# Kernel tuning notes

Hardware: AMD Instinct MI355X
Metric: run time of the kernel (lower is better)

## Reference

```python
import jax, jax.numpy as jnp
import numpy as np

N = 100000      # nodes
E = 1600000     # edges (before self loops)
IN_C, HID_C, OUT_C = 128, 64, 40


def setup_inputs() -> dict:
    key = jax.random.key(0)
    k = jax.random.split(key, 6)
    x = jax.random.normal(k[0], (N, IN_C), dtype=jnp.float32)
    edge_index = jax.random.randint(k[1], (2, E), 0, N, dtype=jnp.int64)
    W1 = jax.random.normal(k[2], (IN_C, HID_C), dtype=jnp.float32) * (1.0 / np.sqrt(IN_C))
    b1 = jnp.zeros((HID_C,), jnp.float32)
    W2 = jax.random.normal(k[3], (HID_C, OUT_C), dtype=jnp.float32) * (1.0 / np.sqrt(HID_C))
    b2 = jnp.zeros((OUT_C,), jnp.float32)
    beta2 = jnp.ones((), jnp.float32)  # learnable beta of prop2 (init 1.0)
    return {"x": x, "edge_index": edge_index, "W1": W1, "b1": b1,
            "W2": W2, "b2": b2, "beta2": beta2}


def _agnn_prop(x, src, dst, beta, n):
    # L2-normalize node features (F.normalize, eps=1e-12 on norm)
    xn = x * jax.lax.rsqrt(jnp.maximum(jnp.sum(x * x, axis=-1, keepdims=True), 1e-24))
    # per-edge cosine similarity scaled by beta
    alpha = beta * jnp.sum(xn[src] * xn[dst], axis=-1)           # [E']
    # scatter-softmax over edges grouped by destination node
    amax = jax.ops.segment_max(alpha, dst, num_segments=n)       # [N]
    e = jnp.exp(alpha - amax[dst])
    denom = jax.ops.segment_sum(e, dst, num_segments=n)          # [N]
    w = e / denom[dst]                                           # [E']
    # gather-weighted aggregation of (unnormalized) source features
    return jax.ops.segment_sum(x[src] * w[:, None], dst, num_segments=n)


def reference(x, edge_index, W1, b1, W2, b2, beta2):
    n = x.shape[0]
    # AGNNConv add_self_loops=True
    loops = jnp.arange(n, dtype=edge_index.dtype)
    src = jnp.concatenate([edge_index[0], loops])
    dst = jnp.concatenate([edge_index[1], loops])
    h = jax.nn.relu(x @ W1 + b1)                                 # [N, HID]
    h = _agnn_prop(h, src, dst, jnp.float32(1.0), n)             # prop1: fixed beta=1
    h = _agnn_prop(h, src, dst, beta2, n)                        # prop2: learnable beta
    logits = h @ W2 + b2                                         # [N, OUT]
    return jax.nn.log_softmax(logits, axis=1)
```

## Files before the change

kernel.cpp:

```cpp
#include <hip/hip_runtime.h>
#include <math.h>

#define INC 128
#define HID 64
#define OUTC 40
#define SHIFT 9
#define MAXB 256
#define NPB 64
#define ONB 96
#define LSW 41
#define SRCM 0x1FFFF
#define PLDS 12288

typedef _Float16 half2_t __attribute__((ext_vector_type(2)));

__device__ inline void fma4(float4& a, float s, const float4& w) {
    a.x += s * w.x; a.y += s * w.y; a.z += s * w.z; a.w += s * w.w;
}
__device__ inline unsigned pkh(float a, float b) {
    unsigned short ua = __builtin_bit_cast(unsigned short, (_Float16)a);
    unsigned short ub = __builtin_bit_cast(unsigned short, (_Float16)b);
    return (unsigned)ua | ((unsigned)ub << 16);
}
__device__ inline float fdot2_(unsigned a, unsigned b, float c) {
#if __has_builtin(__builtin_amdgcn_fdot2)
    return __builtin_amdgcn_fdot2(__builtin_bit_cast(half2_t, a),
                                  __builtin_bit_cast(half2_t, b), c, false);
#else
    half2_t ha = __builtin_bit_cast(half2_t, a);
    half2_t hb = __builtin_bit_cast(half2_t, b);
    return fmaf((float)ha[0], (float)hb[0], fmaf((float)ha[1], (float)hb[1], c));
#endif
}
__device__ inline float dot4(const uint4& a, const uint4& b) {
    float d = fdot2_(a.x, b.x, 0.f);
    d = fdot2_(a.y, b.y, d);
    d = fdot2_(a.z, b.z, d);
    d = fdot2_(a.w, b.w, d);
    return d;
}
__device__ inline void unpack8(float* f, const uint4& a) {
    half2_t p;
    p = __builtin_bit_cast(half2_t, a.x); f[0] = (float)p[0]; f[1] = (float)p[1];
    p = __builtin_bit_cast(half2_t, a.y); f[2] = (float)p[0]; f[3] = (float)p[1];
    p = __builtin_bit_cast(half2_t, a.z); f[4] = (float)p[0]; f[5] = (float)p[1];
    p = __builtin_bit_cast(half2_t, a.w); f[6] = (float)p[0]; f[7] = (float)p[1];
}
__device__ inline void dacc4(float4& a, unsigned xp_, const uint4& w) {
    a.x = fdot2_(xp_, w.x, a.x);
    a.y = fdot2_(xp_, w.y, a.y);
    a.z = fdot2_(xp_, w.z, a.z);
    a.w = fdot2_(xp_, w.w, a.w);
}
__device__ inline void pacc(half2_t* acc, float s, const uint4& a) {
    _Float16 hs = (_Float16)s;
    half2_t s2 = {hs, hs};
    acc[0] += s2 * __builtin_bit_cast(half2_t, a.x);
    acc[1] += s2 * __builtin_bit_cast(half2_t, a.y);
    acc[2] += s2 * __builtin_bit_cast(half2_t, a.z);
    acc[3] += s2 * __builtin_bit_cast(half2_t, a.w);
}
template<int CTRL>
__device__ inline float dppadd(float d) {
    int x = __builtin_amdgcn_update_dpp(0, __builtin_bit_cast(int, d),
                                        CTRL, 0xf, 0xf, true);
    return d + __builtin_bit_cast(float, x);
}
__device__ inline float red8(float d) {
    d = dppadd<0xB1>(d);
    d = dppadd<0x4E>(d);
    d = dppadd<0x141>(d);
    return d;
}
__device__ inline float red16(float d) {
    d = dppadd<0xB1>(d);
    d = dppadd<0x4E>(d);
    d = dppadd<0x141>(d);
    d = dppadd<0x140>(d);
    return d;
}
#define EXP2(x) __builtin_amdgcn_exp2f(x)


__global__ __launch_bounds__(256) void k_hist(const int* __restrict__ ei, int E,
                                              int* __restrict__ bucket_cnt,
                                              int* __restrict__ blk_cnt, int nbuck) {
    __shared__ int lh[MAXB];
    int tid = threadIdx.x;
    for (int i = tid; i < nbuck; i += 256) lh[i] = 0;
    __syncthreads();
    int base = blockIdx.x * 4096;
    int end = min(base + 4096, E);
    for (int e = base + tid; e < end; e += 256)
        atomicAdd(&lh[ei[E + e] >> SHIFT], 1);
    __syncthreads();
    for (int i = tid; i < nbuck; i += 256) {
        int v = lh[i];
        blk_cnt[blockIdx.x * MAXB + i] = v;
        if (v) atomicAdd(&bucket_cnt[i], v);
    }
}

__global__ __launch_bounds__(256) void k_bscan(const int* __restrict__ bucket_cnt,
                                               int* __restrict__ pair_base,
                                               int* __restrict__ pair_fill,
                                               int* __restrict__ row_ptr,
                                               int* __restrict__ csr_src,
                                               int n, int E, int nbuck) {
    __shared__ int tmp[MAXB];
    int tid = threadIdx.x;
    int cnt = (tid < nbuck) ? bucket_cnt[tid] : 0;
    tmp[tid] = cnt;
    __syncthreads();
    for (int off = 1; off < 256; off <<= 1) {
        int t = (tid >= off) ? tmp[tid - off] : 0;
        __syncthreads();
        tmp[tid] += t;
        __syncthreads();
    }
    if (tid < nbuck) { int pb = tmp[tid] - cnt; pair_base[tid] = pb; pair_fill[tid] = pb; }
    if (tid == 0) row_ptr[n] = E;
    if (tid < 16) csr_src[E + tid] = 0;
}

__global__ __launch_bounds__(256) void k_bin(const int* __restrict__ ei, int E,
                                             const int* __restrict__ blk_cnt,
                                             int* __restrict__ pair_fill,
                                             unsigned* __restrict__ pairs, int nbuck) {
    __shared__ int lbase[MAXB];
    int tid = threadIdx.x;
    for (int i = tid; i < nbuck; i += 256) {
        int v = blk_cnt[blockIdx.x * MAXB + i];
        lbase[i] = v ? atomicAdd(&pair_fill[i], v) : 0;
    }
    __syncthreads();
    int base = blockIdx.x * 4096;
    int end = min(base + 4096, E);
    for (int e = base + tid; e < end; e += 256) {
        int s = ei[e], d = ei[E + e];
        int pos = atomicAdd(&lbase[d >> SHIFT], 1);
        pairs[pos] = (unsigned)s | ((unsigned)(d & ((1 << SHIFT) - 1)) << 17);
    }
}

__global__ __launch_bounds__(256) void k_build(const unsigned* __restrict__ pairs,
                                               const int* __restrict__ pair_base,
                                               const int* __restrict__ bucket_cnt,
                                               int* __restrict__ row_ptr,
                                               int* __restrict__ csr_src, int n) {
    __shared__ int cnt[1 << SHIFT];
    __shared__ int offs[1 << SHIFT];
    __shared__ int stmp[256];
    __shared__ unsigned plds[PLDS];
    int b = blockIdx.x;
    int tid = threadIdx.x;
    int nb0 = b << SHIFT;
    int W = min(n - nb0, 1 << SHIFT);
    int p0 = pair_base[b], pc = bucket_cnt[b];
    bool inl = (pc <= PLDS);

    cnt[tid] = 0; cnt[tid + 256] = 0;
    if (inl) for (int i = tid; i < pc; i += 256) plds[i] = pairs[p0 + i];
    __syncthreads();
    if (inl) {
        for (int i = tid; i < pc; i += 256) atomicAdd(&cnt[plds[i] >> 17], 1);
    } else {
        for (int i = tid; i < pc; i += 256) atomicAdd(&cnt[pairs[p0 + i] >> 17], 1);
    }
    __syncthreads();

    int i0 = 2 * tid, i1 = 2 * tid + 1;
    int s0 = (i0 < W) ? cnt[i0] : 0;
    int s1 = (i1 < W) ? cnt[i1] : 0;
    int ps = s0 + s1;
    stmp[tid] = ps;
    __syncthreads();
    for (int off = 1; off < 256; off <<= 1) {
        int t = (tid >= off) ? stmp[tid - off] : 0;
        __syncthreads();
        stmp[tid] += t;
        __syncthreads();
    }
    int excl = stmp[tid] - ps;
    if (i0 < W) { row_ptr[nb0 + i0] = p0 + excl;      offs[i0] = excl; }
    if (i1 < W) { row_ptr[nb0 + i1] = p0 + excl + s0; offs[i1] = excl + s0; }
    __syncthreads();
    if (inl) {
        for (int i = tid; i < pc; i += 256) {
            unsigned pr = plds[i];
            int pos = atomicAdd(&offs[pr >> 17], 1);
            csr_src[p0 + pos] = (int)(pr & SRCM);
        }
    } else {
        for (int i = tid; i < pc; i += 256) {
            unsigned pr = pairs[p0 + i];
            int pos = atomicAdd(&offs[pr >> 17], 1);
            csr_src[p0 + pos] = (int)(pr & SRCM);
        }
    }
}


__global__ __launch_bounds__(256, 4) void k_linear1(const float* __restrict__ x,
                                                    const float* __restrict__ W1,
                                                    const float* __restrict__ b1,
                                                    uint2* __restrict__ X1,
                                                    float* __restrict__ nrm1, int n) {
    __shared__ unsigned Wp[64 * 64];
    __shared__ unsigned xp[64 * 64];
    int tid = threadIdx.x;
    int base = blockIdx.x * NPB;

    for (int t = tid; t < 1024; t += 256) {
        int kp = t >> 4;
        int c4 = t & 15;
        float4 a = ((const float4*)W1)[(2 * kp) * 16 + c4];
        float4 b = ((const float4*)W1)[(2 * kp + 1) * 16 + c4];
        uint4 w;
        w.x = pkh(a.x, b.x); w.y = pkh(a.y, b.y);
        w.z = pkh(a.z, b.z); w.w = pkh(a.w, b.w);
        *(uint4*)&Wp[kp * 64 + c4 * 4] = w;
    }
    for (int t = tid; t < 1024; t += 256) {
        int nl = t >> 4;
        int k8 = t & 15;
        int gn = base + nl;
        float4 a, b;
        if (gn < n) {
            a = ((const float4*)x)[(size_t)gn * 32 + k8 * 2];
            b = ((const float4*)x)[(size_t)gn * 32 + k8 * 2 + 1];
        } else { a = make_float4(0,0,0,0); b = a; }
        uint4 v;
        v.x = pkh(a.x, a.y); v.y = pkh(a.z, a.w);
        v.z = pkh(b.x, b.y); v.w = pkh(b.z, b.w);
        int key = ((nl >> 2) & 3) << 2;
        *(uint4*)&xp[nl * 64 + ((k8 * 4) ^ key)] = v;
    }
    __syncthreads();

    int cg = tid & 15;
    int ng = tid >> 4;
    int n0 = ng * 4;
    const int key = (ng & 3) << 2;
    float4 acc0 = {0,0,0,0}, acc1 = {0,0,0,0}, acc2 = {0,0,0,0}, acc3 = {0,0,0,0};

    #pragma unroll 4
    for (int k4 = 0; k4 < 64; k4 += 4) {
        uint4 xq0 = *(uint4*)&xp[(n0 + 0) * 64 + (k4 ^ key)];
        uint4 xq1 = *(uint4*)&xp[(n0 + 1) * 64 + (k4 ^ key)];
        uint4 xq2 = *(uint4*)&xp[(n0 + 2) * 64 + (k4 ^ key)];
        uint4 xq3 = *(uint4*)&xp[(n0 + 3) * 64 + (k4 ^ key)];
        uint4 wq0 = *(uint4*)&Wp[(k4 + 0) * 64 + cg * 4];
        uint4 wq1 = *(uint4*)&Wp[(k4 + 1) * 64 + cg * 4];
        uint4 wq2 = *(uint4*)&Wp[(k4 + 2) * 64 + cg * 4];
        uint4 wq3 = *(uint4*)&Wp[(k4 + 3) * 64 + cg * 4];
        dacc4(acc0, xq0.x, wq0); dacc4(acc0, xq0.y, wq1); dacc4(acc0, xq0.z, wq2); dacc4(acc0, xq0.w, wq3);
        dacc4(acc1, xq1.x, wq0); dacc4(acc1, xq1.y, wq1); dacc4(acc1, xq1.z, wq2); dacc4(acc1, xq1.w, wq3);
        dacc4(acc2, xq2.x, wq0); dacc4(acc2, xq2.y, wq1); dacc4(acc2, xq2.z, wq2); dacc4(acc2, xq2.w, wq3);
        dacc4(acc3, xq3.x, wq0); dacc4(acc3, xq3.y, wq1); dacc4(acc3, xq3.z, wq2); dacc4(acc3, xq3.w, wq3);
    }

    float4 bb = ((const float4*)b1)[cg];
    float4 r[4] = {acc0, acc1, acc2, acc3};
    #pragma unroll
    for (int nl = 0; nl < 4; ++nl) {
        int node = base + n0 + nl;
        float4 v = r[nl];
        v.x = fmaxf(v.x + bb.x, 0.f); v.y = fmaxf(v.y + bb.y, 0.f);
        v.z = fmaxf(v.z + bb.z, 0.f); v.w = fmaxf(v.w + bb.w, 0.f);
        float q = v.x * v.x + v.y * v.y + v.z * v.z + v.w * v.w;
        q = red16(q);
        float rq = rsqrtf(fmaxf(q, 1e-24f));
        if (node < n) {
            X1[(size_t)node * 16 + cg] = make_uint2(pkh(v.x * rq, v.y * rq),
                                                    pkh(v.z * rq, v.w * rq));
            if (cg == 0) nrm1[node] = sqrtf(fmaxf(q, 1e-24f));
        }
    }
}


template<bool HFOUT>
__global__ __launch_bounds__(256) void k_prop(const uint4* __restrict__ X,
                                              const float* __restrict__ nrm,
                                              const int* __restrict__ row_ptr,
                                              const int* __restrict__ csr_src,
                                              const float* __restrict__ beta_ptr,
                                              uint4* __restrict__ Xout,
                                              float* __restrict__ nrm_out, int n) {
    int node = blockIdx.x * 4 + (threadIdx.x >> 6);
    if (node >= n) return;
    int lane = threadIdx.x & 63;
    int g = lane >> 3, gl = lane & 7;
    float beta = beta_ptr ? beta_ptr[0] : 1.0f;
    float b2 = beta * 1.4426950408889634f;

    uint4 hdp = X[(unsigned)node * 8u + gl];
    int s0 = row_ptr[node], s1 = row_ptr[node + 1];
    float nd = nrm[node];

    float eself = (nd > 1.5e-12f) ? EXP2(b2) : 1.0f;
    float den0 = (g == 0) ? eself : 0.f;
    float den1 = 0.f;
    half2_t acc[4] = {{0,0},{0,0},{0,0},{0,0}};
    pacc(acc, (g == 0) ? eself * nd : 0.f, hdp);

    if (s0 < s1) {
        int i0 = csr_src[s0 + g];
        int i1 = csr_src[s0 + 8 + g];
        uint4 a0 = X[(unsigned)i0 * 8u + gl];
        uint4 a1 = X[(unsigned)i1 * 8u + gl];
        float n0 = nrm[i0], n1 = nrm[i1];
        bool v0 = s0 + g < s1, v1 = s0 + 8 + g < s1;
        for (int j = s0 + 16; j < s1; j += 16) {
            int i0n = csr_src[j + g];
            int i1n = csr_src[j + 8 + g];
            uint4 a0n = X[(unsigned)i0n * 8u + gl];
            uint4 a1n = X[(unsigned)i1n * 8u + gl];
            float n0n = nrm[i0n], n1n = nrm[i1n];
            float d0 = red8(dot4(a0, hdp));
            float d1 = red8(dot4(a1, hdp));
            float e0 = v0 ? EXP2(b2 * d0) : 0.f;
            float e1 = v1 ? EXP2(b2 * d1) : 0.f;
            den0 += e0; den1 += e1;
            pacc(acc, e0 * n0, a0);
            pacc(acc, e1 * n1, a1);
            a0 = a0n; a1 = a1n; n0 = n0n; n1 = n1n;
            v0 = j + g < s1; v1 = j + 8 + g < s1;
        }
        float d0 = red8(dot4(a0, hdp));
        float d1 = red8(dot4(a1, hdp));
        float e0 = v0 ? EXP2(b2 * d0) : 0.f;
        float e1 = v1 ? EXP2(b2 * d1) : 0.f;
        den0 += e0; den1 += e1;
        pacc(acc, e0 * n0, a0);
        pacc(acc, e1 * n1, a1);
    }

    float den = den0 + den1;
    #pragma unroll
    for (int r = 8; r <= 32; r <<= 1) {
        #pragma unroll
        for (int c = 0; c < 4; ++c) {
            unsigned u = __shfl_xor(__builtin_bit_cast(unsigned, acc[c]), r, 64);
            acc[c] += __builtin_bit_cast(half2_t, u);
        }
        den += __shfl_xor(den, r, 64);
    }
    float inv = 1.0f / den;
    float o[8];
    #pragma unroll
    for (int c = 0; c < 4; ++c) {
        o[2 * c]     = (float)acc[c][0] * inv;
        o[2 * c + 1] = (float)acc[c][1] * inv;
    }

    if (HFOUT) {
        float q = 0.f;
        #pragma unroll
        for (int c = 0; c < 8; ++c) q += o[c] * o[c];
        q = red8(q);
        float rq = rsqrtf(fmaxf(q, 1e-24f));
        if (g == 0) {
            uint4 w;
            w.x = pkh(o[0] * rq, o[1] * rq);
            w.y = pkh(o[2] * rq, o[3] * rq);
            w.z = pkh(o[4] * rq, o[5] * rq);
            w.w = pkh(o[6] * rq, o[7] * rq);
            Xout[(unsigned)node * 8u + gl] = w;
            if (gl == 0) nrm_out[node] = sqrtf(fmaxf(q, 1e-24f));
        }
    } else {
        if (g == 0) {
            uint4 w;
            w.x = pkh(o[0], o[1]); w.y = pkh(o[2], o[3]);
            w.z = pkh(o[4], o[5]); w.w = pkh(o[6], o[7]);
            Xout[(unsigned)node * 8u + gl] = w;
        }
    }
}


__global__ __launch_bounds__(256) void k_out(const uint4* __restrict__ Xh,
                                             const float* __restrict__ W2,
                                             const float* __restrict__ b2,
                                             float* __restrict__ out, int n) {
    __shared__ float hs[ONB * HID];
    __shared__ float W2s[HID * OUTC];
    __shared__ float ls[ONB * LSW];
    int tid = threadIdx.x;
    int base = blockIdx.x * ONB;

    for (int i = tid; i < HID * OUTC / 4; i += 256)
        ((float4*)W2s)[i] = ((const float4*)W2)[i];
    for (int i = tid; i < ONB * 8; i += 256) {
        int nl = i >> 3, k8 = i & 7;
        int gn = base + nl;
        uint4 v = (gn < n) ? Xh[(size_t)gn * 8 + k8] : make_uint4(0, 0, 0, 0);
        float f[8]; unpack8(f, v);
        int key = ((nl >> 2) & 7) << 2;
        *(float4*)&hs[nl * HID + ((k8 * 8) ^ key)]     = make_float4(f[0], f[1], f[2], f[3]);
        *(float4*)&hs[nl * HID + ((k8 * 8 + 4) ^ key)] = make_float4(f[4], f[5], f[6], f[7]);
    }
    __syncthreads();

    if (tid < 240) {
        int ng = tid / 10, cg = tid % 10;
        int n0 = ng * 4;
        const int sw = ((ng & 7) << 2);
        float4 acc0 = {0,0,0,0}, acc1 = {0,0,0,0}, acc2 = {0,0,0,0}, acc3 = {0,0,0,0};
        #pragma unroll 4
        for (int k = 0; k < HID; k += 4) {
            float4 w0 = *(float4*)&W2s[(k + 0) * OUTC + cg * 4];
            float4 w1 = *(float4*)&W2s[(k + 1) * OUTC + cg * 4];
            float4 w2 = *(float4*)&W2s[(k + 2) * OUTC + cg * 4];
            float4 w3 = *(float4*)&W2s[(k + 3) * OUTC + cg * 4];
            float4 x0 = *(float4*)&hs[(n0 + 0) * HID + (k ^ sw)];
            float4 x1 = *(float4*)&hs[(n0 + 1) * HID + (k ^ sw)];
            float4 x2 = *(float4*)&hs[(n0 + 2) * HID + (k ^ sw)];
            float4 x3 = *(float4*)&hs[(n0 + 3) * HID + (k ^ sw)];
            fma4(acc0, x0.x, w0); fma4(acc0, x0.y, w1); fma4(acc0, x0.z, w2); fma4(acc0, x0.w, w3);
            fma4(acc1, x1.x, w0); fma4(acc1, x1.y, w1); fma4(acc1, x1.z, w2); fma4(acc1, x1.w, w3);
            fma4(acc2, x2.x, w0); fma4(acc2, x2.y, w1); fma4(acc2, x2.z, w2); fma4(acc2, x2.w, w3);
            fma4(acc3, x3.x, w0); fma4(acc3, x3.y, w1); fma4(acc3, x3.z, w2); fma4(acc3, x3.w, w3);
        }
        float4 bb = ((const float4*)b2)[cg];
        float4 rr[4] = {acc0, acc1, acc2, acc3};
        #pragma unroll
        for (int i = 0; i < 4; ++i) {
            int lb = (n0 + i) * LSW + cg * 4;
            ls[lb + 0] = rr[i].x + bb.x;
            ls[lb + 1] = rr[i].y + bb.y;
            ls[lb + 2] = rr[i].z + bb.z;
            ls[lb + 3] = rr[i].w + bb.w;
        }
    }
    __syncthreads();

    if (tid < ONB) {
        int node = base + tid;
        if (node < n) {
            float m = -INFINITY;
            #pragma unroll
            for (int c = 0; c < OUTC; ++c) m = fmaxf(m, ls[tid * LSW + c]);
            float z = 0.f;
            #pragma unroll
            for (int c = 0; c < OUTC; ++c) z += __expf(ls[tid * LSW + c] - m);
            float lz = m + __logf(z);
            #pragma unroll
            for (int c = 0; c < OUTC; ++c)
                out[(size_t)node * OUTC + c] = ls[tid * LSW + c] - lz;
        }
    }
}


extern "C" void kernel_launch(void* const* d_in, const int* in_sizes, int n_in,
                              void* d_out, int out_size, void* d_ws, size_t ws_size,
                              hipStream_t stream) {
    const float* x   = (const float*)d_in[0];
    const int*   ei  = (const int*)d_in[1];
    const float* W1  = (const float*)d_in[2];
    const float* b1  = (const float*)d_in[3];
    const float* W2  = (const float*)d_in[4];
    const float* b2  = (const float*)d_in[5];
    const float* beta2 = (const float*)d_in[6];
    float* out = (float*)d_out;

    const int n = in_sizes[0] / INC;
    const int E = in_sizes[1] / 2;
    const int nbuck = (n + (1 << SHIFT) - 1) >> SHIFT;
    const int cgrid = (E + 4095) / 4096;

    char* p = (char*)d_ws;
    uint4* X1 = (uint4*)p;             p += (size_t)n * 8 * 16;
    uint4* X2 = (uint4*)p;             p += (size_t)n * 8 * 16;
    uint4* X3 = (uint4*)p;             p += (size_t)n * 8 * 16;
    float* nrm1 = (float*)p;           p += (size_t)n * 4;
    float* nrm2 = (float*)p;           p += (size_t)n * 4;
    int* bucket_cnt  = (int*)p;        p += MAXB * 4;
    int* pair_base   = (int*)p;        p += MAXB * 4;
    int* pair_fill   = (int*)p;        p += MAXB * 4;
    int* row_ptr = (int*)p;            p += (size_t)(n + 1) * 4;
    int* csr_src = (int*)p;            p += (size_t)(E + 16) * 4;
    int* blk_cnt = (int*)p;            p += (size_t)cgrid * MAXB * 4;
    unsigned* pairs = (unsigned*)X3;

    (void)hipMemsetAsync(bucket_cnt, 0, MAXB * 4, stream);
    k_hist<<<cgrid, 256, 0, stream>>>(ei, E, bucket_cnt, blk_cnt, nbuck);
    k_bscan<<<1, 256, 0, stream>>>(bucket_cnt, pair_base, pair_fill, row_ptr, csr_src,
                                   n, E, nbuck);
    k_bin<<<cgrid, 256, 0, stream>>>(ei, E, blk_cnt, pair_fill, pairs, nbuck);
    k_build<<<nbuck, 256, 0, stream>>>(pairs, pair_base, bucket_cnt, row_ptr, csr_src, n);

    k_linear1<<<(n + NPB - 1) / NPB, 256, 0, stream>>>(x, W1, b1, (uint2*)X1, nrm1, n);
    int pgrid = (n + 3) / 4;
    k_prop<true><<<pgrid, 256, 0, stream>>>(X1, nrm1, row_ptr, csr_src, nullptr,
                                            X2, nrm2, n);
    k_prop<false><<<pgrid, 256, 0, stream>>>(X2, nrm2, row_ptr, csr_src, beta2,
                                             X3, nullptr, n);
    k_out<<<(n + ONB - 1) / ONB, 256, 0, stream>>>(X3, W2, b2, out, n);
}
```

Before: 181.0 us.

## Map one 8-lane group per node and process nodes sorted by degree

The propagation kernel now gives each destination node a single 8-lane group instead of a whole 64-lane wavefront, so 32 nodes share a block and the cross-group shuffle reduction goes away. Nodes are counting-sorted by in-degree (a histogram built in k_build, a scan kernel, and a scatter kernel producing an order array), so groups in the same wavefront have similar edge counts and diverge less. The aim is to stop wasting lanes on low-degree nodes (about 17 edges on average) and to shorten the reduction. In exchange, each group walks its edges serially two at a time, and the kernel adds two small launches plus atomic contention on the degree histogram.

```diff
diff --git a/kernel.cpp b/kernel.cpp
--- a/kernel.cpp
+++ b/kernel.cpp
@@ -147,7 +147,8 @@
                                                const int* __restrict__ pair_base,
                                                const int* __restrict__ bucket_cnt,
                                                int* __restrict__ row_ptr,
-                                               int* __restrict__ csr_src, int n) {
+                                               int* __restrict__ csr_src,
+                                               int* __restrict__ dhist, int n) {
     __shared__ int cnt[1 << SHIFT];
     __shared__ int offs[1 << SHIFT];
     __shared__ int stmp[256];
@@ -172,6 +173,8 @@
     int i0 = 2 * tid, i1 = 2 * tid + 1;
     int s0 = (i0 < W) ? cnt[i0] : 0;
     int s1 = (i1 < W) ? cnt[i1] : 0;
+    if (i0 < W) atomicAdd(&dhist[min(s0, 255)], 1);
+    if (i1 < W) atomicAdd(&dhist[min(s1, 255)], 1);
     int ps = s0 + s1;
     stmp[tid] = ps;
     __syncthreads();
@@ -197,6 +200,32 @@
             int pos = atomicAdd(&offs[pr >> 17], 1);
             csr_src[p0 + pos] = (int)(pr & SRCM);
         }
+    }
+}
+
+__global__ void k_dscan(int* __restrict__ dhist) {
+    __shared__ int tmp[256];
+    int tid = threadIdx.x;
+    int v = dhist[tid];
+    tmp[tid] = v;
+    __syncthreads();
+    for (int off = 1; off < 256; off <<= 1) {
+        int t = (tid >= off) ? tmp[tid - off] : 0;
+        __syncthreads();
+        tmp[tid] += t;
+        __syncthreads();
+    }
+    dhist[tid] = tmp[tid] - v;
+}
+
+__global__ __launch_bounds__(256) void k_dscatter(const int* __restrict__ row_ptr,
+                                                  int* __restrict__ dfill,
+                                                  int* __restrict__ order, int n) {
+    int v = blockIdx.x * 256 + threadIdx.x;
+    if (v < n) {
+        int deg = min(row_ptr[v + 1] - row_ptr[v], 255);
+        int pos = atomicAdd(&dfill[deg], 1);
+        order[pos] = v;
     }
 }
 
@@ -285,13 +314,14 @@
                                               const float* __restrict__ nrm,
                                               const int* __restrict__ row_ptr,
                                               const int* __restrict__ csr_src,
+                                              const int* __restrict__ order,
                                               const float* __restrict__ beta_ptr,
                                               uint4* __restrict__ Xout,
                                               float* __restrict__ nrm_out, int n) {
-    int node = blockIdx.x * 4 + (threadIdx.x >> 6);
-    if (node >= n) return;
-    int lane = threadIdx.x & 63;
-    int g = lane >> 3, gl = lane & 7;
+    int gid = (blockIdx.x << 5) + (threadIdx.x >> 3);
+    if (gid >= n) return;
+    int node = order[gid];
+    int gl = threadIdx.x & 7;
     float beta = beta_ptr ? beta_ptr[0] : 1.0f;
     float b2 = beta * 1.4426950408889634f;
 
@@ -300,53 +330,42 @@
     float nd = nrm[node];
 
     float eself = (nd > 1.5e-12f) ? EXP2(b2) : 1.0f;
-    float den0 = (g == 0) ? eself : 0.f;
-    float den1 = 0.f;
+    float den = eself;
     half2_t acc[4] = {{0,0},{0,0},{0,0},{0,0}};
-    pacc(acc, (g == 0) ? eself * nd : 0.f, hdp);
+    pacc(acc, eself * nd, hdp);
 
     if (s0 < s1) {
-        int i0 = csr_src[s0 + g];
-        int i1 = csr_src[s0 + 8 + g];
+        int i0 = csr_src[s0];
+        int i1 = csr_src[s0 + 1];
         uint4 a0 = X[(unsigned)i0 * 8u + gl];
         uint4 a1 = X[(unsigned)i1 * 8u + gl];
         float n0 = nrm[i0], n1 = nrm[i1];
-        bool v0 = s0 + g < s1, v1 = s0 + 8 + g < s1;
-        for (int j = s0 + 16; j < s1; j += 16) {
-            int i0n = csr_src[j + g];
-            int i1n = csr_src[j + 8 + g];
+        bool v1 = s0 + 1 < s1;
+        for (int j = s0 + 2; j < s1; j += 2) {
+            int i0n = csr_src[j];
+            int i1n = csr_src[j + 1];
             uint4 a0n = X[(unsigned)i0n * 8u + gl];
             uint4 a1n = X[(unsigned)i1n * 8u + gl];
             float n0n = nrm[i0n], n1n = nrm[i1n];
             float d0 = red8(dot4(a0, hdp));
             float d1 = red8(dot4(a1, hdp));
-            float e0 = v0 ? EXP2(b2 * d0) : 0.f;
+            float e0 = EXP2(b2 * d0);
             float e1 = v1 ? EXP2(b2 * d1) : 0.f;
-            den0 += e0; den1 += e1;
+            den += e0 + e1;
             pacc(acc, e0 * n0, a0);
             pacc(acc, e1 * n1, a1);
             a0 = a0n; a1 = a1n; n0 = n0n; n1 = n1n;
-            v0 = j + g < s1; v1 = j + 8 + g < s1;
+            v1 = j + 1 < s1;
         }
         float d0 = red8(dot4(a0, hdp));
         float d1 = red8(dot4(a1, hdp));
-        float e0 = v0 ? EXP2(b2 * d0) : 0.f;
+        float e0 = EXP2(b2 * d0);
         float e1 = v1 ? EXP2(b2 * d1) : 0.f;
-        den0 += e0; den1 += e1;
+        den += e0 + e1;
         pacc(acc, e0 * n0, a0);
         pacc(acc, e1 * n1, a1);
     }
 
-    float den = den0 + den1;
-    #pragma unroll
-    for (int r = 8; r <= 32; r <<= 1) {
-        #pragma unroll
-        for (int c = 0; c < 4; ++c) {
-            unsigned u = __shfl_xor(__builtin_bit_cast(unsigned, acc[c]), r, 64);
-            acc[c] += __builtin_bit_cast(half2_t, u);
-        }
-        den += __shfl_xor(den, r, 64);
-    }
     float inv = 1.0f / den;
     float o[8];
     #pragma unroll
@@ -361,22 +380,18 @@
         for (int c = 0; c < 8; ++c) q += o[c] * o[c];
         q = red8(q);
         float rq = rsqrtf(fmaxf(q, 1e-24f));
-        if (g == 0) {
-            uint4 w;
-            w.x = pkh(o[0] * rq, o[1] * rq);
-            w.y = pkh(o[2] * rq, o[3] * rq);
-            w.z = pkh(o[4] * rq, o[5] * rq);
-            w.w = pkh(o[6] * rq, o[7] * rq);
-            Xout[(unsigned)node * 8u + gl] = w;
-            if (gl == 0) nrm_out[node] = sqrtf(fmaxf(q, 1e-24f));
-        }
+        uint4 w;
+        w.x = pkh(o[0] * rq, o[1] * rq);
+        w.y = pkh(o[2] * rq, o[3] * rq);
+        w.z = pkh(o[4] * rq, o[5] * rq);
+        w.w = pkh(o[6] * rq, o[7] * rq);
+        Xout[(unsigned)node * 8u + gl] = w;
+        if (gl == 0) nrm_out[node] = sqrtf(fmaxf(q, 1e-24f));
     } else {
-        if (g == 0) {
-            uint4 w;
-            w.x = pkh(o[0], o[1]); w.y = pkh(o[2], o[3]);
-            w.z = pkh(o[4], o[5]); w.w = pkh(o[6], o[7]);
-            Xout[(unsigned)node * 8u + gl] = w;
-        }
+        uint4 w;
+        w.x = pkh(o[0], o[1]); w.y = pkh(o[2], o[3]);
+        w.z = pkh(o[4], o[5]); w.w = pkh(o[6], o[7]);
+        Xout[(unsigned)node * 8u + gl] = w;
     }
 }
 
@@ -478,7 +493,9 @@
     uint4* X3 = (uint4*)p;             p += (size_t)n * 8 * 16;
     float* nrm1 = (float*)p;           p += (size_t)n * 4;
     float* nrm2 = (float*)p;           p += (size_t)n * 4;
+    int* order = (int*)p;              p += (size_t)n * 4;
     int* bucket_cnt  = (int*)p;        p += MAXB * 4;
+    int* dhist       = (int*)p;        p += 256 * 4;
     int* pair_base   = (int*)p;        p += MAXB * 4;
     int* pair_fill   = (int*)p;        p += MAXB * 4;
     int* row_ptr = (int*)p;            p += (size_t)(n + 1) * 4;
@@ -486,18 +503,21 @@
     int* blk_cnt = (int*)p;            p += (size_t)cgrid * MAXB * 4;
     unsigned* pairs = (unsigned*)X3;
 
-    (void)hipMemsetAsync(bucket_cnt, 0, MAXB * 4, stream);
+    (void)hipMemsetAsync(bucket_cnt, 0, (MAXB + 256) * 4, stream);
     k_hist<<<cgrid, 256, 0, stream>>>(ei, E, bucket_cnt, blk_cnt, nbuck);
     k_bscan<<<1, 256, 0, stream>>>(bucket_cnt, pair_base, pair_fill, row_ptr, csr_src,
                                    n, E, nbuck);
     k_bin<<<cgrid, 256, 0, stream>>>(ei, E, blk_cnt, pair_fill, pairs, nbuck);
-    k_build<<<nbuck, 256, 0, stream>>>(pairs, pair_base, bucket_cnt, row_ptr, csr_src, n);
+    k_build<<<nbuck, 256, 0, stream>>>(pairs, pair_base, bucket_cnt, row_ptr, csr_src,
+                                       dhist, n);
+    k_dscan<<<1, 256, 0, stream>>>(dhist);
+    k_dscatter<<<(n + 255) / 256, 256, 0, stream>>>(row_ptr, dhist, order, n);
 
     k_linear1<<<(n + NPB - 1) / NPB, 256, 0, stream>>>(x, W1, b1, (uint2*)X1, nrm1, n);
-    int pgrid = (n + 3) / 4;
-    k_prop<true><<<pgrid, 256, 0, stream>>>(X1, nrm1, row_ptr, csr_src, nullptr,
+    int pgrid = (n + 31) / 32;
+    k_prop<true><<<pgrid, 256, 0, stream>>>(X1, nrm1, row_ptr, csr_src, order, nullptr,
                                             X2, nrm2, n);
-    k_prop<false><<<pgrid, 256, 0, stream>>>(X2, nrm2, row_ptr, csr_src, beta2,
+    k_prop<false><<<pgrid, 256, 0, stream>>>(X2, nrm2, row_ptr, csr_src, order, beta2,
                                              X3, nullptr, n);
     k_out<<<(n + ONB - 1) / ONB, 256, 0, stream>>>(X3, W2, b2, out, n);
 }
```

New measurement: 703.2 us. 3.88x slower.
